# Performance work log

Measured on AMD Instinct MI355X. Metric: run time of the kernel, lower is better.

## Reference

```python
import jax, jax.numpy as jnp
import numpy as np

B, L, D, N = 4, 2048, 1024, 8
H = D // N  # head_dim = 128
EPS = 1e-6


def _ln(x, gamma, beta, axes):
    m = jnp.mean(x, axis=axes, keepdims=True)
    v = jnp.mean(jnp.square(x - m), axis=axes, keepdims=True)
    return (x - m) * jax.lax.rsqrt(v + EPS) * gamma + beta


def setup_inputs() -> dict:
    key = jax.random.key(0)
    ks = jax.random.split(key, 8)
    glorot_d = (6.0 / (D + D)) ** 0.5  # GlorotUniform over fan_in=D, fan_out=N*H=D
    inputs = jax.random.normal(ks[0], (B, L, D), dtype=jnp.float32)
    attention_mask = jnp.tril(jnp.ones((L, L), dtype=bool))[None].repeat(B, axis=0)
    return {
        'inputs': inputs,
        'attention_mask': attention_mask,
        'ln_in_gamma': jnp.ones((D,), jnp.float32),
        'ln_in_beta': jnp.zeros((D,), jnp.float32),
        'wu': jax.random.uniform(ks[1], (D, N, H), jnp.float32, -glorot_d, glorot_d),
        'wq': jax.random.uniform(ks[2], (D, N, H), jnp.float32, -glorot_d, glorot_d),
        'wk': jax.random.uniform(ks[3], (D, N, H), jnp.float32, -glorot_d, glorot_d),
        'wv': jax.random.uniform(ks[4], (D, N, H), jnp.float32, -glorot_d, glorot_d),
        'ln_attn_gamma': jnp.ones((N, H), jnp.float32),
        'ln_attn_beta': jnp.zeros((N, H), jnp.float32),
        'wo': jax.random.uniform(ks[5], (N, H, D), jnp.float32, -glorot_d, glorot_d),
    }


def reference(inputs, attention_mask, ln_in_gamma, ln_in_beta, wu, wq, wk, wv,
              ln_attn_gamma, ln_attn_beta, wo):
    x = _ln(inputs, ln_in_gamma, ln_in_beta, axes=-1)  # [B,L,D]
    u = jax.nn.silu(jnp.einsum('btd,dnh->btnh', x, wu))
    q = jax.nn.silu(jnp.einsum('btd,dnh->btnh', x, wq))
    k = jax.nn.silu(jnp.einsum('btd,dnh->btnh', x, wk))
    v = jax.nn.silu(jnp.einsum('btd,dnh->btnh', x, wv))
    # pointwise silu attention, normalized by sequence length
    qk = jnp.einsum('bthd,bshd->bhts', q, k)  # [B,N,L,L]
    seq_len = q.shape[1]
    attn = jax.nn.silu(qk) / seq_len
    attn = jnp.where(attention_mask[:, None, :, :], attn, 0.0)
    attn_out = jnp.einsum('bhts,bshd->bthd', attn, v)  # [B,L,N,H]
    normed = _ln(attn_out, ln_attn_gamma, ln_attn_beta, axes=(-2, -1))
    out = jnp.einsum('btnh,nhd->btd', u * normed, wo)
    return out + inputs
```

## Files before the change

kernel.cpp:

```cpp
#include <hip/hip_runtime.h>
#include <hip/hip_bf16.h>
#include <stdint.h>

#define D_    1024
#define L_    2048
#define B_    4
#define NHEAD 8
#define HDIM  128
#define BL_   (B_*L_)
#define EPS_  1e-6f

typedef __attribute__((ext_vector_type(8))) short short8;
typedef __attribute__((ext_vector_type(4))) float f32x4;

__device__ __forceinline__ unsigned short f2bf(float f) {
  unsigned u = __builtin_bit_cast(unsigned, f);
  unsigned r = 0x7fffu + ((u >> 16) & 1u);
  return (unsigned short)((u + r) >> 16);
}
__device__ __forceinline__ float bf2f(unsigned short h) {
  return __builtin_bit_cast(float, ((unsigned)h) << 16);
}
__device__ __forceinline__ float silu_f(float x) {
  return x * __builtin_amdgcn_rcpf(1.f + __expf(-x));
}
__device__ __forceinline__ unsigned cvt_pk_bf16(float lo, float hi) {
  unsigned r;
  asm("v_cvt_pk_bf16_f32 %0, %1, %2" : "=v"(r) : "v"(lo), "v"(hi));
  return r;
}

__device__ __forceinline__ void gll16(const void* g, void* l) {
  auto gp = reinterpret_cast<const __attribute__((address_space(1))) unsigned*>(
      reinterpret_cast<uintptr_t>(g));
  auto lp = reinterpret_cast<__attribute__((address_space(3))) unsigned*>(
      (unsigned)reinterpret_cast<uintptr_t>(l));
  __builtin_amdgcn_global_load_lds(gp, lp, 16, 0, 0);
}

__global__ __launch_bounds__(256) void wt_kernel(
    const float* __restrict__ wu, const float* __restrict__ wq,
    const float* __restrict__ wk, const float* __restrict__ wv,
    const float* __restrict__ wo, unsigned short* __restrict__ wt)
{
  __shared__ float t[64][65];
  int mat = blockIdx.z;
  const float* src = mat==0?wu: mat==1?wq: mat==2?wk: mat==3?wv: wo;
  unsigned short* dst = wt + (size_t)mat*D_*D_;
  int r0 = blockIdx.y*64, c0 = blockIdx.x*64;
  int tid = threadIdx.x;
  for (int i = 0; i < 16; ++i) {
    int e = i*256 + tid; int r = e>>6, c = e&63;
    t[r][c] = src[(size_t)(r0+r)*D_ + c0 + c];
  }
  __syncthreads();
  for (int i = 0; i < 16; ++i) {
    int e = i*256 + tid; int r = e>>6, c = e&63;
    dst[(size_t)(c0+r)*D_ + r0 + c] = f2bf(t[c][r]);
  }
}

__global__ __launch_bounds__(256) void ln_in_kernel(
    const float* __restrict__ in, const float* __restrict__ gamma,
    const float* __restrict__ beta, unsigned short* __restrict__ x)
{
  int row = blockIdx.x, tid = threadIdx.x;
  float4 v = ((const float4*)(in + (size_t)row*D_))[tid];
  float s = v.x+v.y+v.z+v.w;
  float ss = v.x*v.x + v.y*v.y + v.z*v.z + v.w*v.w;
  #pragma unroll
  for (int o = 32; o; o >>= 1) { s += __shfl_down(s,o); ss += __shfl_down(ss,o); }
  __shared__ float red[8];
  int lane = tid&63, wid = tid>>6;
  if (lane==0) { red[wid]=s; red[4+wid]=ss; }
  __syncthreads();
  s = red[0]+red[1]+red[2]+red[3];
  ss = red[4]+red[5]+red[6]+red[7];
  float mean = s * (1.f/D_);
  float var  = ss * (1.f/D_) - mean*mean;
  float rstd = rsqrtf(var + EPS_);
  float4 g = ((const float4*)gamma)[tid], b = ((const float4*)beta)[tid];
  ushort4 o;
  o.x = f2bf((v.x-mean)*rstd*g.x + b.x);
  o.y = f2bf((v.y-mean)*rstd*g.y + b.y);
  o.z = f2bf((v.z-mean)*rstd*g.z + b.z);
  o.w = f2bf((v.w-mean)*rstd*g.w + b.w);
  ((ushort4*)(x + (size_t)row*D_))[tid] = o;
}

template<int MODE>
__global__ __launch_bounds__(512) __attribute__((amdgpu_waves_per_eu(2,2))) void gemm8p(
    const unsigned short* __restrict__ A, const unsigned short* __restrict__ Bt,
    unsigned short* __restrict__ o_u, unsigned short* __restrict__ o_q,
    unsigned short* __restrict__ o_k, unsigned short* __restrict__ o_vt,
    const float* __restrict__ resid, float* __restrict__ o_f)
{
  constexpr int BN  = (MODE==0) ? 256 : 128;
  constexpr int WN  = (MODE==0) ? 4 : 2;
  constexpr int WTM = (MODE==0) ? 128 : 64;
  constexpr int MF  = WTM/16;
  constexpr int BNS = BN*32;
  constexpr int BOFF = 32768;
  constexpr int RG  = BN/64;
  constexpr int NBCHW = (BNS/512)/8;
  const int K = 1024;

  __shared__ unsigned short lds[BOFF + 4*BNS];

  int lane = threadIdx.x & 63, wid = threadIdx.x >> 6;
  int wr = wid / WN, wc = wid % WN;
  int m0 = blockIdx.x * 256;
  int n0 = blockIdx.y * BN;
  const unsigned short* Ab = A + (size_t)m0*K;
  const unsigned short* Bb = Bt + (size_t)n0*K;

  f32x4 acc[MF][4] = {};

  auto stage = [&](int dbs, int k0) {
    #pragma unroll
    for (int j = 0; j < 2; ++j) {
      int c = wid*2 + j;
      int row = (c&3)*64 + lane;
      int kof = k0 + ((c>>2)<<3);
      gll16(Ab + (size_t)row*K + kof, &lds[dbs*8192 + c*512]);
    }
    #pragma unroll
    for (int j = 0; j < NBCHW; ++j) {
      int c = wid*NBCHW + j;
      int kk8 = c / RG, rg = c % RG;
      int row = rg*64 + lane;
      int kof = k0 + (kk8<<3);
      gll16(Bb + (size_t)row*K + kof, &lds[BOFF + dbs*BNS + c*512]);
    }
  };

  #pragma unroll
  for (int gp = 0; gp < 4; ++gp) stage(gp, gp*32);
  if constexpr (MODE==0) asm volatile("s_waitcnt vmcnt(12)" ::: "memory");
  else                   asm volatile("s_waitcnt vmcnt(9)"  ::: "memory");
  __builtin_amdgcn_s_barrier();

  auto do_phase = [&](int g, bool dostage) {
    const int bs = g & 3;
    const int kk4 = lane>>4, l15 = lane&15;
    short8 af[MF], bfr[4];
    const int ab = bs*8192 + kk4*2048 + (wr*WTM + l15)*8;
    #pragma unroll
    for (int m = 0; m < MF; ++m) af[m] = *(const short8*)&lds[ab + m*128];
    const int bb = BOFF + bs*BNS + kk4*(BN*8) + (wc*64 + l15)*8;
    #pragma unroll
    for (int n = 0; n < 4; ++n) bfr[n] = *(const short8*)&lds[bb + n*128];
    if (dostage) {
      int tp = g + 3;
      int k0 = (tp < 32 ? tp : 31) * 32;
      stage(tp & 3, k0);
    }
    __builtin_amdgcn_sched_barrier(0);
    __builtin_amdgcn_s_barrier();
    asm volatile("s_waitcnt lgkmcnt(0)" ::: "memory");
    __builtin_amdgcn_sched_barrier(0);
    __builtin_amdgcn_s_setprio(1);
    #pragma unroll
    for (int m = 0; m < MF; ++m)
      #pragma unroll
      for (int n = 0; n < 4; ++n)
        acc[m][n] = __builtin_amdgcn_mfma_f32_16x16x32_bf16(af[m], bfr[n], acc[m][n], 0,0,0);
    __builtin_amdgcn_s_setprio(0);
    if constexpr (MODE==0) asm volatile("s_waitcnt vmcnt(8)" ::: "memory");
    else                   asm volatile("s_waitcnt vmcnt(6)" ::: "memory");
    __builtin_amdgcn_sched_barrier(0);
    __builtin_amdgcn_s_barrier();
  };

  do_phase(0, false);
  #pragma unroll
  for (int g = 1; g < 32; ++g) do_phase(g, true);

  if constexpr (MODE == 0) {
    int mat = n0 >> 10;
    int jb = n0 & 1023;
    #pragma unroll
    for (int m = 0; m < MF; ++m) {
      int t_ = m0 + wr*WTM + m*16 + ((lane>>4)<<2);
      #pragma unroll
      for (int n = 0; n < 4; ++n) {
        int jj = jb + wc*64 + n*16 + (lane&15);
        float p0 = silu_f(acc[m][n][0]);
        float p1 = silu_f(acc[m][n][1]);
        float p2 = silu_f(acc[m][n][2]);
        float p3 = silu_f(acc[m][n][3]);
        if (mat == 3) {
          int b = t_ >> 11, tt = t_ & 2047;
          int nn = jj >> 7, h = jj & 127;
          ushort4 pk;
          pk.x = f2bf(p0); pk.y = f2bf(p1); pk.z = f2bf(p2); pk.w = f2bf(p3);
          *(ushort4*)&o_vt[(((size_t)(b*NHEAD+nn))*HDIM + h)*L_ + tt] = pk;
        } else {
          unsigned short* dst = mat==0 ? o_u : (mat==1 ? o_q : o_k);
          dst[(size_t)(t_+0)*D_ + jj] = f2bf(p0);
          dst[(size_t)(t_+1)*D_ + jj] = f2bf(p1);
          dst[(size_t)(t_+2)*D_ + jj] = f2bf(p2);
          dst[(size_t)(t_+3)*D_ + jj] = f2bf(p3);
        }
      }
    }
  } else {
    #pragma unroll
    for (int m = 0; m < MF; ++m) {
      int t_ = m0 + wr*WTM + m*16 + ((lane>>4)<<2);
      #pragma unroll
      for (int n = 0; n < 4; ++n) {
        int jj = n0 + wc*64 + n*16 + (lane&15);
        #pragma unroll
        for (int r = 0; r < 4; ++r)
          o_f[(size_t)(t_+r)*D_ + jj] = acc[m][n][r] + resid[(size_t)(t_+r)*D_ + jj];
      }
    }
  }
}

__global__ __launch_bounds__(512) __attribute__((amdgpu_waves_per_eu(2,2))) void attn_kernel(
    const unsigned short* __restrict__ gq, const unsigned short* __restrict__ gk,
    const unsigned short* __restrict__ gvt, unsigned short* __restrict__ attn_out)
{
  __shared__ unsigned short SM[49152];
  int id = blockIdx.x;
  int x = id & 7, c2 = (id >> 3) & 3, q = id >> 5;
  int bh = 8*c2 + x;
  int b = bh >> 3, n = bh & 7;
  const unsigned short* qb = gq + (size_t)b*L_*D_ + n*HDIM;
  const unsigned short* kb = gk + (size_t)b*L_*D_ + n*HDIM;
  const unsigned short* vb = gvt + (size_t)bh*HDIM*L_;
  unsigned short* ob = attn_out + (size_t)b*L_*D_ + n*HDIM;
  int lane = threadIdx.x & 63, wid = threadIdx.x >> 6;
  int wsel = wid >> 2, wq = wid & 3;
  int wr = wq >> 1, wc = wq & 1;
  int hi = lane >> 4, l15 = lane & 15;
  unsigned short* Kbuf = SM + (wsel ? 8192 : 0);
  unsigned short* Vbuf = SM + 16384 + (wsel ? 8192 : 0);
  unsigned short* Pbuf = SM + 32768 + (wsel ? 8192 : 0);
  unsigned short* Qbuf = SM + 32768;
  float* Cbuf = (float*)SM;

  for (int uu = 0; uu < 2; ++uu) {
    int ti = uu ? q : (15 - q);
    int t0 = ti * 128;
    #pragma unroll
    for (int i = 0; i < 4; ++i) {
      int cc = wid*4 + i;
      gll16(qb + (size_t)(t0 + ((cc&1)<<6) + lane)*D_ + ((cc>>1)<<3), &Qbuf[cc*512]);
    }
    __syncthreads();
    short8 qf[4][4];
    #pragma unroll
    for (int kk = 0; kk < 4; ++kk) {
      int kbase = (kk*4 + hi)*1024;
      #pragma unroll
      for (int fn = 0; fn < 4; ++fn)
        qf[kk][fn] = *(const short8*)&Qbuf[kbase + (wc*64 + fn*16 + l15)*8];
    }
    __syncthreads();
    #pragma unroll
    for (int i = 0; i < 4; ++i) {
      int cc = wq*4 + i;
      gll16(kb + (size_t)(wsel*64 + lane)*D_ + (cc<<3), &Kbuf[cc*512]);
      gll16(vb + (size_t)(((cc&1)<<6) + lane)*L_ + wsel*64 + ((cc>>1)<<3), &Vbuf[cc*512]);
    }
    __syncthreads();

    f32x4 oacc[4][4] = {};
    for (int j = 0; j <= ti; ++j) {
      bool stg = (j < ti);
      int cnext = 2*(j+1) + wsel;
      f32x4 sacc[2][4] = {};
      __builtin_amdgcn_s_setprio(1);
      #pragma unroll
      for (int kk = 0; kk < 4; ++kk) {
        int kbase = (kk*4 + hi)*512;
        short8 kf[2];
        #pragma unroll
        for (int fm = 0; fm < 2; ++fm)
          kf[fm] = *(const short8*)&Kbuf[kbase + (wr*32 + fm*16 + l15)*8];
        #pragma unroll
        for (int fm = 0; fm < 2; ++fm)
          #pragma unroll
          for (int fn = 0; fn < 4; ++fn)
            sacc[fm][fn] = __builtin_amdgcn_mfma_f32_16x16x32_bf16(kf[fm], qf[kk][fn], sacc[fm][fn], 0,0,0);
      }
      __builtin_amdgcn_s_setprio(0);
      uint4 kreg[4];
      if (stg) {
        #pragma unroll
        for (int i = 0; i < 4; ++i) {
          int cc = wq*4 + i;
          kreg[i] = *(const uint4*)(kb + (size_t)(cnext*64 + lane)*D_ + (cc<<3));
        }
      }
      {
        bool diag = (j == ti);
        int maskoff = wsel*64;
        #pragma unroll
        for (int fm = 0; fm < 2; ++fm) {
          int sb = wr*32 + fm*16 + (hi<<2);
          #pragma unroll
          for (int fn = 0; fn < 4; ++fn) {
            int tl = wc*64 + fn*16 + l15;
            float pv[4];
            #pragma unroll
            for (int r = 0; r < 4; ++r) {
              float sv = silu_f(sacc[fm][fn][r]) * (1.f/2048.f);
              if (diag && (tl < maskoff + sb + r)) sv = 0.f;
              pv[r] = sv;
            }
            int a0 = (sb>>3)*1024 + tl*8 + (sb&7);
            *(unsigned*)&Pbuf[a0]   = cvt_pk_bf16(pv[0], pv[1]);
            *(unsigned*)&Pbuf[a0+2] = cvt_pk_bf16(pv[2], pv[3]);
          }
        }
      }
      asm volatile("s_waitcnt vmcnt(0) lgkmcnt(0)" ::: "memory");
      __builtin_amdgcn_sched_barrier(0);
      __builtin_amdgcn_s_barrier();
      __builtin_amdgcn_sched_barrier(0);
      if (stg) {
        #pragma unroll
        for (int i = 0; i < 4; ++i) {
          int cc = wq*4 + i;
          *(uint4*)&Kbuf[cc*512 + lane*8] = kreg[i];
        }
      }
      __builtin_amdgcn_s_setprio(1);
      #pragma unroll
      for (int kk = 0; kk < 2; ++kk) {
        int kbase = (kk*4 + hi)*1024;
        short8 pa[4], vf[4];
        #pragma unroll
        for (int fm = 0; fm < 4; ++fm)
          pa[fm] = *(const short8*)&Pbuf[kbase + (wr*64 + fm*16 + l15)*8];
        #pragma unroll
        for (int fn = 0; fn < 4; ++fn)
          vf[fn] = *(const short8*)&Vbuf[kbase + (wc*64 + fn*16 + l15)*8];
        #pragma unroll
        for (int fm = 0; fm < 4; ++fm)
          #pragma unroll
          for (int fn = 0; fn < 4; ++fn)
            oacc[fm][fn] = __builtin_amdgcn_mfma_f32_16x16x32_bf16(pa[fm], vf[fn], oacc[fm][fn], 0,0,0);
      }
      __builtin_amdgcn_s_setprio(0);
      asm volatile("s_waitcnt lgkmcnt(0)" ::: "memory");
      __builtin_amdgcn_sched_barrier(0);
      __builtin_amdgcn_s_barrier();
      __builtin_amdgcn_sched_barrier(0);
      if (stg) {
        #pragma unroll
        for (int i = 0; i < 4; ++i) {
          int cc = wq*4 + i;
          gll16(vb + (size_t)(((cc&1)<<6) + lane)*L_ + cnext*64 + ((cc>>1)<<3), &Vbuf[cc*512]);
        }
        __builtin_amdgcn_sched_barrier(0);
      }
    }
    if (wsel == 1) {
      #pragma unroll
      for (int fm = 0; fm < 4; ++fm) {
        int tl = wr*64 + fm*16 + (hi<<2);
        #pragma unroll
        for (int fn = 0; fn < 4; ++fn) {
          int h = wc*64 + fn*16 + l15;
          #pragma unroll
          for (int r = 0; r < 4; ++r)
            Cbuf[(tl+r)*128 + h] = oacc[fm][fn][r];
        }
      }
    }
    asm volatile("s_waitcnt lgkmcnt(0)" ::: "memory");
    __builtin_amdgcn_s_barrier();
    __builtin_amdgcn_sched_barrier(0);
    if (wsel == 0) {
      #pragma unroll
      for (int fm = 0; fm < 4; ++fm) {
        int tl = wr*64 + fm*16 + (hi<<2);
        #pragma unroll
        for (int fn = 0; fn < 4; ++fn) {
          int h = wc*64 + fn*16 + l15;
          #pragma unroll
          for (int r = 0; r < 4; ++r) {
            float v = oacc[fm][fn][r] + Cbuf[(tl+r)*128 + h];
            ob[(size_t)(t0 + tl + r)*D_ + h] = f2bf(v);
          }
        }
      }
    }
    __syncthreads();
  }
}

__global__ __launch_bounds__(256) void ln_mul_kernel(
    const unsigned short* __restrict__ ain, const float* __restrict__ gamma,
    const float* __restrict__ beta, const unsigned short* __restrict__ u,
    unsigned short* __restrict__ y)
{
  int row = blockIdx.x, tid = threadIdx.x;
  ushort4 av = ((const ushort4*)(ain + (size_t)row*D_))[tid];
  float v0 = bf2f(av.x), v1 = bf2f(av.y), v2 = bf2f(av.z), v3 = bf2f(av.w);
  float s = v0+v1+v2+v3;
  float ss = v0*v0+v1*v1+v2*v2+v3*v3;
  #pragma unroll
  for (int o = 32; o; o >>= 1) { s += __shfl_down(s,o); ss += __shfl_down(ss,o); }
  __shared__ float red[8];
  int lane = tid&63, wid = tid>>6;
  if (lane==0) { red[wid]=s; red[4+wid]=ss; }
  __syncthreads();
  s = red[0]+red[1]+red[2]+red[3];
  ss = red[4]+red[5]+red[6]+red[7];
  float mean = s * (1.f/D_);
  float var  = ss * (1.f/D_) - mean*mean;
  float rstd = rsqrtf(var + EPS_);
  float4 g = ((const float4*)gamma)[tid], b = ((const float4*)beta)[tid];
  ushort4 uu = ((const ushort4*)(u + (size_t)row*D_))[tid];
  ushort4 o;
  o.x = f2bf(bf2f(uu.x) * ((v0-mean)*rstd*g.x + b.x));
  o.y = f2bf(bf2f(uu.y) * ((v1-mean)*rstd*g.y + b.y));
  o.z = f2bf(bf2f(uu.z) * ((v2-mean)*rstd*g.z + b.z));
  o.w = f2bf(bf2f(uu.w) * ((v3-mean)*rstd*g.w + b.w));
  ((ushort4*)(y + (size_t)row*D_))[tid] = o;
}

extern "C" void kernel_launch(void* const* d_in, const int* in_sizes, int n_in,
                              void* d_out, int out_size, void* d_ws, size_t ws_size,
                              hipStream_t stream) {
  const float* inputs = (const float*)d_in[0];
  const float* g_in = (const float*)d_in[2];
  const float* b_in = (const float*)d_in[3];
  const float* wu = (const float*)d_in[4];
  const float* wq = (const float*)d_in[5];
  const float* wk = (const float*)d_in[6];
  const float* wv = (const float*)d_in[7];
  const float* g_at = (const float*)d_in[8];
  const float* b_at = (const float*)d_in[9];
  const float* wo = (const float*)d_in[10];
  float* out = (float*)d_out;

  char* ws = (char*)d_ws;
  unsigned short* x   = (unsigned short*)(ws + ((size_t)0));
  unsigned short* q   = (unsigned short*)(ws + ((size_t)16<<20));
  unsigned short* k   = (unsigned short*)(ws + ((size_t)32<<20));
  unsigned short* u   = (unsigned short*)(ws + ((size_t)48<<20));
  unsigned short* vt  = (unsigned short*)(ws + ((size_t)64<<20));
  unsigned short* wt  = (unsigned short*)(ws + ((size_t)80<<20));
  unsigned short* ao  = (unsigned short*)(ws + ((size_t)96<<20));
  unsigned short* y = x;

  wt_kernel<<<dim3(16,16,5), 256, 0, stream>>>(wu, wq, wk, wv, wo, wt);
  ln_in_kernel<<<BL_, 256, 0, stream>>>(inputs, g_in, b_in, x);
  gemm8p<0><<<dim3(32,16), 512, 0, stream>>>(x, wt, u, q, k, vt, nullptr, nullptr);
  attn_kernel<<<256, 512, 0, stream>>>(q, k, vt, ao);
  ln_mul_kernel<<<BL_, 256, 0, stream>>>(ao, g_at, b_at, u, y);
  gemm8p<1><<<dim3(32,8), 512, 0, stream>>>(y, wt + (size_t)4*D_*D_,
                                            nullptr, nullptr, nullptr, nullptr, inputs, out);
}
```

Baseline: 257.0 us.

## Restructure GEMM mainloop into double-buffered 64-wide K tiles with split sub-phases

Replaces the 4-stage ring of 32-wide K slices with a 2-buffer scheme over 64-wide K tiles. Each tile is processed in four sub-phases that interleave staging of the next tile's A/B halves with MFMA work. The warp layout becomes fixed 2x4 for both GEMM modes, so the output-projection GEMM now uses 8x2 fragments per wave. Fewer barriers per K and larger loads per stage aim to cut synchronization overhead, but the shallower prefetch depth and the full vmcnt(0) wait each tile may expose memory latency.

```diff
diff --git a/kernel.cpp b/kernel.cpp
--- a/kernel.cpp
+++ b/kernel.cpp
@@ -96,95 +96,145 @@
     const float* __restrict__ resid, float* __restrict__ o_f)
 {
   constexpr int BN  = (MODE==0) ? 256 : 128;
-  constexpr int WN  = (MODE==0) ? 4 : 2;
-  constexpr int WTM = (MODE==0) ? 128 : 64;
-  constexpr int MF  = WTM/16;
-  constexpr int BNS = BN*32;
-  constexpr int BOFF = 32768;
-  constexpr int RG  = BN/64;
-  constexpr int NBCHW = (BNS/512)/8;
+  constexpr int NF  = BN/64;
+  constexpr int BDS = BN*64;
   const int K = 1024;
 
-  __shared__ unsigned short lds[BOFF + 4*BNS];
+  __shared__ unsigned short lds[32768 + 2*BDS];
 
   int lane = threadIdx.x & 63, wid = threadIdx.x >> 6;
-  int wr = wid / WN, wc = wid % WN;
+  int wr = wid >> 2, wc = wid & 3;
+  int hi = lane >> 4, l15 = lane & 15;
   int m0 = blockIdx.x * 256;
   int n0 = blockIdx.y * BN;
   const unsigned short* Ab = A + (size_t)m0*K;
   const unsigned short* Bb = Bt + (size_t)n0*K;
 
-  f32x4 acc[MF][4] = {};
-
-  auto stage = [&](int dbs, int k0) {
+  f32x4 acc[8][NF] = {};
+  short8 bfr_[NF];
+
+  auto stageA = [&](int d, int t1, int h) {
     #pragma unroll
     for (int j = 0; j < 2; ++j) {
-      int c = wid*2 + j;
-      int row = (c&3)*64 + lane;
-      int kof = k0 + ((c>>2)<<3);
-      gll16(Ab + (size_t)row*K + kof, &lds[dbs*8192 + c*512]);
-    }
-    #pragma unroll
-    for (int j = 0; j < NBCHW; ++j) {
-      int c = wid*NBCHW + j;
-      int kk8 = c / RG, rg = c % RG;
-      int row = rg*64 + lane;
-      int kof = k0 + (kk8<<3);
-      gll16(Bb + (size_t)row*K + kof, &lds[BOFF + dbs*BNS + c*512]);
+      int c = wid*2 + j, k8 = c>>1, rh = c&1;
+      gll16(Ab + (size_t)(h*128 + rh*64 + lane)*K + t1*64 + k8*8,
+            &lds[d*16384 + (k8*256 + h*128 + rh*64)*8]);
     }
   };
-
-  #pragma unroll
-  for (int gp = 0; gp < 4; ++gp) stage(gp, gp*32);
-  if constexpr (MODE==0) asm volatile("s_waitcnt vmcnt(12)" ::: "memory");
-  else                   asm volatile("s_waitcnt vmcnt(9)"  ::: "memory");
+  auto stageB = [&](int d, int t1, int h) {
+    if constexpr (MODE==0) {
+      #pragma unroll
+      for (int j = 0; j < 2; ++j) {
+        int c = wid*2 + j, k8 = c>>1, ch = c&1;
+        gll16(Bb + (size_t)(h*128 + ch*64 + lane)*K + t1*64 + k8*8,
+              &lds[32768 + d*16384 + (k8*256 + h*128 + ch*64)*8]);
+      }
+    } else {
+      gll16(Bb + (size_t)(h*64 + lane)*K + t1*64 + wid*8,
+            &lds[32768 + d*8192 + (wid*128 + h*64)*8]);
+    }
+  };
+
+#define AFR(m_, kk_) (*(const short8*)&lds[d*16384 + (((kk_)*4+hi)*256 + wr*128 + (m_)*16 + l15)*8])
+#define BFRD(n_, kk_) (*(const short8*)&lds[32768 + d*BDS + (((kk_)*4+hi)*BN + wc*(BN/4) + (n_)*16 + l15)*8])
+
+  stageA(0,0,0); stageA(0,0,1); stageB(0,0,0); stageB(0,0,1);
+  asm volatile("s_waitcnt vmcnt(0)" ::: "memory");
   __builtin_amdgcn_s_barrier();
 
-  auto do_phase = [&](int g, bool dostage) {
-    const int bs = g & 3;
-    const int kk4 = lane>>4, l15 = lane&15;
-    short8 af[MF], bfr[4];
-    const int ab = bs*8192 + kk4*2048 + (wr*WTM + l15)*8;
-    #pragma unroll
-    for (int m = 0; m < MF; ++m) af[m] = *(const short8*)&lds[ab + m*128];
-    const int bb = BOFF + bs*BNS + kk4*(BN*8) + (wc*64 + l15)*8;
-    #pragma unroll
-    for (int n = 0; n < 4; ++n) bfr[n] = *(const short8*)&lds[bb + n*128];
-    if (dostage) {
-      int tp = g + 3;
-      int k0 = (tp < 32 ? tp : 31) * 32;
-      stage(tp & 3, k0);
-    }
-    __builtin_amdgcn_sched_barrier(0);
-    __builtin_amdgcn_s_barrier();
-    asm volatile("s_waitcnt lgkmcnt(0)" ::: "memory");
-    __builtin_amdgcn_sched_barrier(0);
-    __builtin_amdgcn_s_setprio(1);
-    #pragma unroll
-    for (int m = 0; m < MF; ++m)
-      #pragma unroll
-      for (int n = 0; n < 4; ++n)
-        acc[m][n] = __builtin_amdgcn_mfma_f32_16x16x32_bf16(af[m], bfr[n], acc[m][n], 0,0,0);
-    __builtin_amdgcn_s_setprio(0);
-    if constexpr (MODE==0) asm volatile("s_waitcnt vmcnt(8)" ::: "memory");
-    else                   asm volatile("s_waitcnt vmcnt(6)" ::: "memory");
-    __builtin_amdgcn_sched_barrier(0);
-    __builtin_amdgcn_s_barrier();
-  };
-
-  do_phase(0, false);
-  #pragma unroll
-  for (int g = 1; g < 32; ++g) do_phase(g, true);
+  #pragma unroll 2
+  for (int t = 0; t < 16; ++t) {
+    const int d = t & 1;
+    const bool st = (t < 15);
+    {
+      #pragma unroll
+      for (int n = 0; n < NF; ++n) bfr_[n] = BFRD(n, 0);
+      short8 af_[4];
+      #pragma unroll
+      for (int i = 0; i < 4; ++i) af_[i] = AFR(i, 0);
+      if (st) stageA(d^1, t+1, 0);
+      __builtin_amdgcn_s_barrier();
+      asm volatile("s_waitcnt lgkmcnt(0)" ::: "memory");
+      __builtin_amdgcn_sched_barrier(0);
+      __builtin_amdgcn_s_setprio(1);
+      #pragma unroll
+      for (int i = 0; i < 4; ++i)
+        #pragma unroll
+        for (int n = 0; n < NF; ++n)
+          acc[i][n] = __builtin_amdgcn_mfma_f32_16x16x32_bf16(af_[i], bfr_[n], acc[i][n], 0,0,0);
+      __builtin_amdgcn_s_setprio(0);
+      __builtin_amdgcn_sched_barrier(0);
+      __builtin_amdgcn_s_barrier();
+    }
+    {
+      short8 af_[4];
+      #pragma unroll
+      for (int i = 0; i < 4; ++i) af_[i] = AFR(4+i, 0);
+      if (st) { stageA(d^1, t+1, 1); stageB(d^1, t+1, 0); }
+      __builtin_amdgcn_s_barrier();
+      asm volatile("s_waitcnt lgkmcnt(0)" ::: "memory");
+      __builtin_amdgcn_sched_barrier(0);
+      __builtin_amdgcn_s_setprio(1);
+      #pragma unroll
+      for (int i = 0; i < 4; ++i)
+        #pragma unroll
+        for (int n = 0; n < NF; ++n)
+          acc[4+i][n] = __builtin_amdgcn_mfma_f32_16x16x32_bf16(af_[i], bfr_[n], acc[4+i][n], 0,0,0);
+      __builtin_amdgcn_s_setprio(0);
+      __builtin_amdgcn_sched_barrier(0);
+      __builtin_amdgcn_s_barrier();
+    }
+    {
+      #pragma unroll
+      for (int n = 0; n < NF; ++n) bfr_[n] = BFRD(n, 1);
+      short8 af_[4];
+      #pragma unroll
+      for (int i = 0; i < 4; ++i) af_[i] = AFR(i, 1);
+      if (st) stageB(d^1, t+1, 1);
+      __builtin_amdgcn_s_barrier();
+      asm volatile("s_waitcnt lgkmcnt(0)" ::: "memory");
+      __builtin_amdgcn_sched_barrier(0);
+      __builtin_amdgcn_s_setprio(1);
+      #pragma unroll
+      for (int i = 0; i < 4; ++i)
+        #pragma unroll
+        for (int n = 0; n < NF; ++n)
+          acc[i][n] = __builtin_amdgcn_mfma_f32_16x16x32_bf16(af_[i], bfr_[n], acc[i][n], 0,0,0);
+      __builtin_amdgcn_s_setprio(0);
+      __builtin_amdgcn_sched_barrier(0);
+      __builtin_amdgcn_s_barrier();
+    }
+    {
+      short8 af_[4];
+      #pragma unroll
+      for (int i = 0; i < 4; ++i) af_[i] = AFR(4+i, 1);
+      __builtin_amdgcn_s_barrier();
+      asm volatile("s_waitcnt lgkmcnt(0)" ::: "memory");
+      __builtin_amdgcn_sched_barrier(0);
+      __builtin_amdgcn_s_setprio(1);
+      #pragma unroll
+      for (int i = 0; i < 4; ++i)
+        #pragma unroll
+        for (int n = 0; n < NF; ++n)
+          acc[4+i][n] = __builtin_amdgcn_mfma_f32_16x16x32_bf16(af_[i], bfr_[n], acc[4+i][n], 0,0,0);
+      __builtin_amdgcn_s_setprio(0);
+      asm volatile("s_waitcnt vmcnt(0)" ::: "memory");
+      __builtin_amdgcn_sched_barrier(0);
+      __builtin_amdgcn_s_barrier();
+    }
+  }
+#undef AFR
+#undef BFRD
 
   if constexpr (MODE == 0) {
     int mat = n0 >> 10;
     int jb = n0 & 1023;
     #pragma unroll
-    for (int m = 0; m < MF; ++m) {
-      int t_ = m0 + wr*WTM + m*16 + ((lane>>4)<<2);
-      #pragma unroll
-      for (int n = 0; n < 4; ++n) {
-        int jj = jb + wc*64 + n*16 + (lane&15);
+    for (int m = 0; m < 8; ++m) {
+      int t_ = m0 + wr*128 + m*16 + (hi<<2);
+      #pragma unroll
+      for (int n = 0; n < NF; ++n) {
+        int jj = jb + wc*64 + n*16 + l15;
         float p0 = silu_f(acc[m][n][0]);
         float p1 = silu_f(acc[m][n][1]);
         float p2 = silu_f(acc[m][n][2]);
@@ -206,11 +256,11 @@
     }
   } else {
     #pragma unroll
-    for (int m = 0; m < MF; ++m) {
-      int t_ = m0 + wr*WTM + m*16 + ((lane>>4)<<2);
-      #pragma unroll
-      for (int n = 0; n < 4; ++n) {
-        int jj = n0 + wc*64 + n*16 + (lane&15);
+    for (int m = 0; m < 8; ++m) {
+      int t_ = m0 + wr*128 + m*16 + (hi<<2);
+      #pragma unroll
+      for (int n = 0; n < NF; ++n) {
+        int jj = n0 + wc*32 + n*16 + l15;
         #pragma unroll
         for (int r = 0; r < 4; ++r)
           o_f[(size_t)(t_+r)*D_ + jj] = acc[m][n][r] + resid[(size_t)(t_+r)*D_ + jj];
```

Measured after the change: 249.2 us. -3.0%, faster.
